# Kernel optimization log

Measured on AMD Instinct MI355X. Metric: run time of the kernel, lower is better.

Reference implementation:

```python
import math
import jax, jax.numpy as jnp
from jax import lax
import numpy as np

BLEND_RATIO = 0.15


def _cosine_window(h, w, br):
    # numpy: static shapes, matches torch _cosine_window
    yh = max(1, int(round(h * br)))
    xw = max(1, int(round(w * br)))
    y = np.ones((h, 1), dtype=np.float64)
    ty = np.linspace(0.0, math.pi, yh)
    fy = 0.5 * (1.0 - np.cos(ty))
    y[:yh, 0] = fy
    y[-yh:, 0] = fy[::-1]
    x = np.ones((1, w), dtype=np.float64)
    tx = np.linspace(0.0, math.pi, xw)
    fx = 0.5 * (1.0 - np.cos(tx))
    x[0, :xw] = fx
    x[0, -xw:] = fx[::-1]
    return np.clip(y @ x, 1e-6, 1.0)


def setup_inputs() -> dict:
    key = jax.random.key(0)
    k1, k2 = jax.random.split(key)
    x = jax.random.normal(k1, (8, 3, 1024, 1024), dtype=jnp.float32)
    kernels = jax.random.uniform(k2, (4, 4, 15, 15), dtype=jnp.float32)
    return {"x": x, "kernels": kernels}


def reference(x, kernels):
    b, c, H, W = x.shape
    ny, nx, K, _ = kernels.shape
    pad = K // 2
    hh = [H // ny + (1 if y < H % ny else 0) for y in range(ny)]
    ww = [W // nx + (1 if i < W % nx else 0) for i in range(nx)]
    y0 = [0]
    for h in hh[:-1]:
        y0.append(y0[-1] + h)
    x0 = [0]
    for w in ww[:-1]:
        x0.append(x0[-1] + w)

    out = jnp.zeros_like(x)
    acc = jnp.zeros((b, 1, H, W), dtype=x.dtype)
    for j in range(ny):
        for i in range(nx):
            h, w = hh[j], ww[i]
            ys, xs = y0[j], x0[i]
            k = kernels[j, i]
            k = k / (k.sum() + 1e-12)
            # depthwise weight (c, 1, K, K)
            wgt = jnp.broadcast_to(k[None, None], (c, 1, K, K))
            patch = lax.dynamic_slice(x, (0, 0, ys, xs), (b, c, h, w))
            padded = jnp.pad(patch, ((0, 0), (0, 0), (pad, pad), (pad, pad)), mode="edge")
            y_hat = lax.conv_general_dilated(
                padded, wgt, window_strides=(1, 1), padding="VALID",
                dimension_numbers=("NCHW", "OIHW", "NCHW"), feature_group_count=c)
            wmask = jnp.asarray(_cosine_window(h, w, BLEND_RATIO), dtype=x.dtype)  # (h, w)
            out = out.at[:, :, ys:ys + h, xs:xs + w].add(y_hat * wmask[None, None])
            acc = acc.at[:, :, ys:ys + h, xs:xs + w].add(
                jnp.broadcast_to(wmask[None, None], (b, 1, h, w)))
    return out / jnp.clip(acc, 1e-6, None)
```

## Files before the change

### kernel.cpp

```cpp
#include <hip/hip_runtime.h>

#define HH    1024
#define WW    1024
#define KS    15
#define PAD   7
#define CELL  256
#define BX    64
#define TROWS 142
#define TCOLS 80
#define NITER 16
#define CHN   18
#define AWS_CELL_BYTES (KS * 1024)

typedef _Float16     f16x8 __attribute__((ext_vector_type(8)));
typedef _Float16     f16x4 __attribute__((ext_vector_type(4)));
typedef float        f32x4 __attribute__((ext_vector_type(4)));
typedef unsigned int u32x4 __attribute__((ext_vector_type(4)));

static __device__ __forceinline__ void light_barrier() {
    asm volatile("s_waitcnt lgkmcnt(0)\n\ts_barrier" ::: "memory");
}

__global__ __launch_bounds__(256) void pb_prep_kernel(
    const float* __restrict__ kern, unsigned int* __restrict__ aws)
{
    const int cell = blockIdx.x;
    const int tid  = threadIdx.x;
    const int lane = tid & 63;
    const float* kp = kern + cell * (KS * KS);

    float s = 0.f;
    #pragma unroll
    for (int i = 0; i < 4; ++i) {
        int t = lane + 64 * i;
        s += (t < KS * KS) ? kp[t] : 0.f;
    }
    #pragma unroll
    for (int m = 1; m < 64; m <<= 1) s += __shfl_xor(s, m, 64);
    const float inv = 1.0f / (s + 1e-12f);

    const int i  = tid >> 4;
    const int k2 = tid & 15;
    unsigned int* wp = aws + cell * (AWS_CELL_BYTES / 4) + tid;

    for (int dy = 0; dy < KS; ++dy) {
        float v0 = 0.f, v1 = 0.f;
        int dx0 = 2 * k2 - i - 1;
        int dx1 = dx0 + 1;
        if (dx0 >= 0 && dx0 < KS) v0 = kp[dy * KS + dx0] * inv;
        if (dx1 >= 0 && dx1 < KS) v1 = kp[dy * KS + dx1] * inv;
        f16x4 h; h[0] = (_Float16)v0; h[1] = (_Float16)v1; h[2] = 0; h[3] = 0;
        unsigned long long u = __builtin_bit_cast(unsigned long long, h);
        wp[dy * 256] = (unsigned int)u;
    }
}

__global__ __launch_bounds__(256, 4) void pb_mfma_kernel(
    const float* __restrict__ x,
    const unsigned int* __restrict__ aws,
    float* __restrict__ out)
{
    __shared__ __align__(16) _Float16 s_tile[TROWS * TCOLS];

    const int tid  = threadIdx.x;
    const int lane = tid & 63;
    const int w    = tid >> 6;
    const int g    = lane >> 4;
    const int cc   = lane & 15;

    const int bx0 = blockIdx.x * BX;
    const int ci  = blockIdx.x >> 2;
    const int cj  = blockIdx.y;
    const int bc  = blockIdx.z;

    const int cellx0 = ci * CELL;
    const int celly0 = cj * CELL, celly1 = celly0 + CELL - 1;

    const float* plane = x + (size_t)bc * HH * WW;

    const u32x4* ap = (const u32x4*)(aws + (cj * 4 + ci) * (AWS_CELL_BYTES / 4))
                      + cc * 4 + g;
    u32x4 af[KS];
    #pragma unroll
    for (int dy = 0; dy < KS; ++dy) af[dy] = ap[dy * 64];
    #pragma unroll
    for (int dy = 0; dy < KS; ++dy) asm volatile("" : "+v"(af[dy]));

    auto stage_addr = [&](int strip, int lc, int idx) -> const float* {
        int r20  = idx / 20;
        int c4   = idx - r20 * 20;
        int row  = lc * 16 + r20;
        int gy   = min(max(celly0 + strip * 128 - PAD + row, celly0), celly1);
        int gx0  = bx0 - 8 + 4 * c4;
        int gx0c = min(max(gx0, cellx0), cellx0 + CELL - 4);
        return plane + (size_t)gy * WW + gx0c;
    };
    auto write_group = [&](int lc, int idx, float4 v) {
        int r20 = idx / 20;
        int c4  = idx - r20 * 20;
        int row = lc * 16 + r20;
        int gx0 = bx0 - 8 + 4 * c4;
        bool lo = gx0 <  cellx0;
        bool hi = gx0 >  cellx0 + CELL - 4;
        float e0 = hi ? v.w : v.x;
        float e1 = lo ? v.x : (hi ? v.w : v.y);
        float e2 = lo ? v.x : (hi ? v.w : v.z);
        float e3 = lo ? v.x : v.w;
        f16x4 h;
        h[0] = (_Float16)e0; h[1] = (_Float16)e1;
        h[2] = (_Float16)e2; h[3] = (_Float16)e3;
        *(f16x4*)(s_tile + row * TCOLS + 4 * c4) = h;
    };

    float4 n0, n1; bool hn1;
    auto issue_chunk = [&](int c) {
        int strip = c >= 9;
        int lc    = c - 9 * strip;
        int ng    = (lc == 8) ? 280 : 320;
        n0  = *(const float4*)stage_addr(strip, lc, tid);
        hn1 = 256 + tid < ng;
        if (hn1) n1 = *(const float4*)stage_addr(strip, lc, 256 + tid);
    };
    auto write_pending = [&](int c) {
        int strip = c >= 9;
        int lc    = c - 9 * strip;
        (void)strip;
        write_group(lc, tid, n0);
        if (hn1) write_group(lc, 256 + tid, n1);
    };

    issue_chunk(0); write_pending(0);
    issue_chunk(1); write_pending(1);
    issue_chunk(2); write_pending(2);
    issue_chunk(3);
    light_barrier();

    const _Float16* bbase = s_tile + cc * TCOLS + w * 16 + g * 8;
    float* oplane = out + (size_t)bc * HH * WW;

    #pragma unroll
    for (int t = 0; t < NITER; ++t) {
        const int strip = t >> 3;
        const int jpl   = t & 7;

        if (t + 3 < CHN) write_pending(t + 3);
        if (t + 4 < CHN) issue_chunk(t + 4);

        f32x4 acc0 = {0.f, 0.f, 0.f, 0.f};
        f32x4 acc1 = {0.f, 0.f, 0.f, 0.f};
        #pragma unroll
        for (int dy = 0; dy < KS; ++dy) {
            f16x8 b = *(const f16x8*)(bbase + (16 * jpl + dy) * TCOLS);
            if (dy & 1)
                acc1 = __builtin_amdgcn_mfma_f32_16x16x32_f16(
                           __builtin_bit_cast(f16x8, af[dy]), b, acc1, 0, 0, 0);
            else
                acc0 = __builtin_amdgcn_mfma_f32_16x16x32_f16(
                           __builtin_bit_cast(f16x8, af[dy]), b, acc0, 0, 0, 0);
        }
        f32x4 r = acc0 + acc1;
        float* op = oplane
                  + (size_t)(celly0 + strip * 128 + 16 * jpl + cc) * WW
                  + bx0 + 16 * w + 4 * g;
        *(f32x4*)op = r;

        light_barrier();
    }
}

extern "C" void kernel_launch(void* const* d_in, const int* in_sizes, int n_in,
                              void* d_out, int out_size, void* d_ws, size_t ws_size,
                              hipStream_t stream) {
    (void)in_sizes; (void)n_in; (void)ws_size; (void)out_size;
    const float* x    = (const float*)d_in[0];
    const float* kern = (const float*)d_in[1];
    float* out        = (float*)d_out;
    unsigned int* aws = (unsigned int*)d_ws;

    pb_prep_kernel<<<16, 256, 0, stream>>>(kern, aws);
    dim3 grid(WW / BX, 4, 8 * 3);
    pb_mfma_kernel<<<grid, 256, 0, stream>>>(x, aws, out);
}
```

Measured before the change: 58.16 us.

## Specialize a producer wave for tile staging with LDS flag handshakes

Adds a fifth wave per block that alone loads input chunks from global memory, converts them to half precision and writes the shared tile. It signals readiness through per-chunk LDS flags, while the four MFMA waves spin on those flags and publish their progress instead of using block-wide barriers. The goal is to decouple load latency from compute and remove the per-iteration barrier. The cost is that a single wave now issues all staging traffic, and spin-waiting adds overhead and occupancy pressure.

```diff
diff --git a/kernel.cpp b/kernel.cpp
--- a/kernel.cpp
+++ b/kernel.cpp
@@ -17,10 +17,6 @@
 typedef float        f32x4 __attribute__((ext_vector_type(4)));
 typedef unsigned int u32x4 __attribute__((ext_vector_type(4)));
 
-static __device__ __forceinline__ void light_barrier() {
-    asm volatile("s_waitcnt lgkmcnt(0)\n\ts_barrier" ::: "memory");
-}
-
 __global__ __launch_bounds__(256) void pb_prep_kernel(
     const float* __restrict__ kern, unsigned int* __restrict__ aws)
 {
@@ -55,18 +51,18 @@
     }
 }
 
-__global__ __launch_bounds__(256, 4) void pb_mfma_kernel(
+__global__ __launch_bounds__(320, 4) void pb_mfma_kernel(
     const float* __restrict__ x,
     const unsigned int* __restrict__ aws,
     float* __restrict__ out)
 {
     __shared__ __align__(16) _Float16 s_tile[TROWS * TCOLS];
+    __shared__ int s_flag[CHN];
+    __shared__ int s_prog[4];
 
     const int tid  = threadIdx.x;
     const int lane = tid & 63;
-    const int w    = tid >> 6;
-    const int g    = lane >> 4;
-    const int cc   = lane & 15;
+    const int wid  = tid >> 6;
 
     const int bx0 = blockIdx.x * BX;
     const int ci  = blockIdx.x >> 2;
@@ -78,93 +74,134 @@
 
     const float* plane = x + (size_t)bc * HH * WW;
 
-    const u32x4* ap = (const u32x4*)(aws + (cj * 4 + ci) * (AWS_CELL_BYTES / 4))
-                      + cc * 4 + g;
-    u32x4 af[KS];
-    #pragma unroll
-    for (int dy = 0; dy < KS; ++dy) af[dy] = ap[dy * 64];
-    #pragma unroll
-    for (int dy = 0; dy < KS; ++dy) asm volatile("" : "+v"(af[dy]));
-
-    auto stage_addr = [&](int strip, int lc, int idx) -> const float* {
-        int r20  = idx / 20;
-        int c4   = idx - r20 * 20;
-        int row  = lc * 16 + r20;
-        int gy   = min(max(celly0 + strip * 128 - PAD + row, celly0), celly1);
-        int gx0  = bx0 - 8 + 4 * c4;
-        int gx0c = min(max(gx0, cellx0), cellx0 + CELL - 4);
-        return plane + (size_t)gy * WW + gx0c;
-    };
-    auto write_group = [&](int lc, int idx, float4 v) {
-        int r20 = idx / 20;
-        int c4  = idx - r20 * 20;
-        int row = lc * 16 + r20;
-        int gx0 = bx0 - 8 + 4 * c4;
-        bool lo = gx0 <  cellx0;
-        bool hi = gx0 >  cellx0 + CELL - 4;
-        float e0 = hi ? v.w : v.x;
-        float e1 = lo ? v.x : (hi ? v.w : v.y);
-        float e2 = lo ? v.x : (hi ? v.w : v.z);
-        float e3 = lo ? v.x : v.w;
-        f16x4 h;
-        h[0] = (_Float16)e0; h[1] = (_Float16)e1;
-        h[2] = (_Float16)e2; h[3] = (_Float16)e3;
-        *(f16x4*)(s_tile + row * TCOLS + 4 * c4) = h;
-    };
-
-    float4 n0, n1; bool hn1;
-    auto issue_chunk = [&](int c) {
-        int strip = c >= 9;
-        int lc    = c - 9 * strip;
-        int ng    = (lc == 8) ? 280 : 320;
-        n0  = *(const float4*)stage_addr(strip, lc, tid);
-        hn1 = 256 + tid < ng;
-        if (hn1) n1 = *(const float4*)stage_addr(strip, lc, 256 + tid);
-    };
-    auto write_pending = [&](int c) {
-        int strip = c >= 9;
-        int lc    = c - 9 * strip;
-        (void)strip;
-        write_group(lc, tid, n0);
-        if (hn1) write_group(lc, 256 + tid, n1);
-    };
-
-    issue_chunk(0); write_pending(0);
-    issue_chunk(1); write_pending(1);
-    issue_chunk(2); write_pending(2);
-    issue_chunk(3);
-    light_barrier();
-
-    const _Float16* bbase = s_tile + cc * TCOLS + w * 16 + g * 8;
-    float* oplane = out + (size_t)bc * HH * WW;
-
-    #pragma unroll
-    for (int t = 0; t < NITER; ++t) {
-        const int strip = t >> 3;
-        const int jpl   = t & 7;
-
-        if (t + 3 < CHN) write_pending(t + 3);
-        if (t + 4 < CHN) issue_chunk(t + 4);
-
-        f32x4 acc0 = {0.f, 0.f, 0.f, 0.f};
-        f32x4 acc1 = {0.f, 0.f, 0.f, 0.f};
-        #pragma unroll
-        for (int dy = 0; dy < KS; ++dy) {
-            f16x8 b = *(const f16x8*)(bbase + (16 * jpl + dy) * TCOLS);
-            if (dy & 1)
-                acc1 = __builtin_amdgcn_mfma_f32_16x16x32_f16(
-                           __builtin_bit_cast(f16x8, af[dy]), b, acc1, 0, 0, 0);
-            else
-                acc0 = __builtin_amdgcn_mfma_f32_16x16x32_f16(
-                           __builtin_bit_cast(f16x8, af[dy]), b, acc0, 0, 0, 0);
+    if (tid < CHN) s_flag[tid] = 0;
+    if (tid >= CHN && tid < CHN + 4) s_prog[tid - CHN] = 0;
+    __syncthreads();
+
+    volatile int* vflag = s_flag;
+    volatile int* vprog = s_prog;
+
+    if (wid == 4) {
+        auto stage_addr = [&](int strip, int lc, int gl) -> const float* {
+            int r20  = gl / 20;
+            int c4   = gl - r20 * 20;
+            int row  = lc * 16 + r20;
+            int gy   = min(max(celly0 + strip * 128 - PAD + row, celly0), celly1);
+            int gx0  = bx0 - 8 + 4 * c4;
+            int gx0c = min(max(gx0, cellx0), cellx0 + CELL - 4);
+            return plane + (size_t)gy * WW + gx0c;
+        };
+        auto write_group = [&](int lc, int gl, float4 v) {
+            int r20 = gl / 20;
+            int c4  = gl - r20 * 20;
+            int row = lc * 16 + r20;
+            int gx0 = bx0 - 8 + 4 * c4;
+            bool lo = gx0 <  cellx0;
+            bool hi = gx0 >  cellx0 + CELL - 4;
+            float e0 = hi ? v.w : v.x;
+            float e1 = lo ? v.x : (hi ? v.w : v.y);
+            float e2 = lo ? v.x : (hi ? v.w : v.z);
+            float e3 = lo ? v.x : v.w;
+            f16x4 h;
+            h[0] = (_Float16)e0; h[1] = (_Float16)e1;
+            h[2] = (_Float16)e2; h[3] = (_Float16)e3;
+            *(f16x4*)(s_tile + row * TCOLS + 4 * c4) = h;
+        };
+
+        float4 bufA[5], bufB[5];
+        bool   hA[5], hB[5];
+
+        {
+            #pragma unroll
+            for (int i = 0; i < 5; ++i) {
+                int gl = lane + 64 * i;
+                hA[i] = gl < 320;
+                if (hA[i]) bufA[i] = *(const float4*)stage_addr(0, 0, gl);
+            }
         }
-        f32x4 r = acc0 + acc1;
-        float* op = oplane
-                  + (size_t)(celly0 + strip * 128 + 16 * jpl + cc) * WW
-                  + bx0 + 16 * w + 4 * g;
-        *(f32x4*)op = r;
-
-        light_barrier();
+        #pragma unroll
+        for (int c = 0; c < CHN; ++c) {
+            const bool slotA  = (c & 1) == 0;
+            if (c + 1 < CHN) {
+                const int c1     = c + 1;
+                const int strip1 = c1 >= 9;
+                const int lc1    = c1 - 9 * strip1;
+                const int ng1    = (lc1 == 8) ? 280 : 320;
+                #pragma unroll
+                for (int i = 0; i < 5; ++i) {
+                    int gl = lane + 64 * i;
+                    bool h = gl < ng1;
+                    if (slotA) { hB[i] = h; if (h) bufB[i] = *(const float4*)stage_addr(strip1, lc1, gl); }
+                    else       { hA[i] = h; if (h) bufA[i] = *(const float4*)stage_addr(strip1, lc1, gl); }
+                }
+            }
+            {
+                const int strip = c >= 9;
+                const int lc    = c - 9 * strip;
+                if (c >= 9) {
+                    const int need = lc + 1;
+                    for (;;) {
+                        int m0 = vprog[0], m1 = vprog[1];
+                        int m2 = vprog[2], m3 = vprog[3];
+                        if (min(min(m0, m1), min(m2, m3)) >= need) break;
+                        __builtin_amdgcn_s_sleep(8);
+                    }
+                }
+                #pragma unroll
+                for (int i = 0; i < 5; ++i) {
+                    int gl = lane + 64 * i;
+                    if (slotA) { if (hA[i]) write_group(lc, gl, bufA[i]); }
+                    else       { if (hB[i]) write_group(lc, gl, bufB[i]); }
+                }
+                asm volatile("s_waitcnt lgkmcnt(0)" ::: "memory");
+                if (lane == 0) vflag[c] = 1;
+            }
+        }
+    } else {
+        const int w  = wid;
+        const int g  = lane >> 4;
+        const int cc = lane & 15;
+
+        const u32x4* ap = (const u32x4*)(aws + (cj * 4 + ci) * (AWS_CELL_BYTES / 4))
+                          + cc * 4 + g;
+        u32x4 af[KS];
+        #pragma unroll
+        for (int dy = 0; dy < KS; ++dy) af[dy] = ap[dy * 64];
+        #pragma unroll
+        for (int dy = 0; dy < KS; ++dy) asm volatile("" : "+v"(af[dy]));
+
+        const _Float16* bbase = s_tile + cc * TCOLS + w * 16 + g * 8;
+        float* oplane = out + (size_t)bc * HH * WW;
+
+        #pragma unroll
+        for (int t = 0; t < NITER; ++t) {
+            const int strip = t >> 3;
+            const int jpl   = t & 7;
+            const int lastc = 9 * strip + jpl + 1;
+
+            while (vflag[lastc] == 0) __builtin_amdgcn_s_sleep(2);
+
+            f32x4 acc0 = {0.f, 0.f, 0.f, 0.f};
+            f32x4 acc1 = {0.f, 0.f, 0.f, 0.f};
+            #pragma unroll
+            for (int dy = 0; dy < KS; ++dy) {
+                f16x8 b = *(const f16x8*)(bbase + (16 * jpl + dy) * TCOLS);
+                if (dy & 1)
+                    acc1 = __builtin_amdgcn_mfma_f32_16x16x32_f16(
+                               __builtin_bit_cast(f16x8, af[dy]), b, acc1, 0, 0, 0);
+                else
+                    acc0 = __builtin_amdgcn_mfma_f32_16x16x32_f16(
+                               __builtin_bit_cast(f16x8, af[dy]), b, acc0, 0, 0, 0);
+            }
+            f32x4 r = acc0 + acc1;
+            float* op = oplane
+                      + (size_t)(celly0 + strip * 128 + 16 * jpl + cc) * WW
+                      + bx0 + 16 * w + 4 * g;
+            *(f32x4*)op = r;
+
+            asm volatile("s_waitcnt lgkmcnt(0)" ::: "memory");
+            if (lane == 0) vprog[w] = t + 1;
+        }
     }
 }
 
@@ -179,5 +216,5 @@
 
     pb_prep_kernel<<<16, 256, 0, stream>>>(kern, aws);
     dim3 grid(WW / BX, 4, 8 * 3);
-    pb_mfma_kernel<<<grid, 256, 0, stream>>>(x, aws, out);
+    pb_mfma_kernel<<<grid, 320, 0, stream>>>(x, aws, out);
 }
```

Result: slower. 61.80 us (+6.2%).
